# Kernel optimization log

Measured on AMD Instinct MI355X. Metric: run time of the kernel, lower is better.

The kernel has to match this reference:

```python
import jax, jax.numpy as jnp
import numpy as np
import math

EMBED_DIM = 768
NUM_HEADS = 12
HEAD_DIM = EMBED_DIM // NUM_HEADS
B, L = 8, 1024


def setup_inputs() -> dict:
    key = jax.random.key(0)
    ks = jax.random.split(key, 10)
    s = 1.0 / math.sqrt(EMBED_DIM)
    x = jax.random.normal(ks[0], (B, L, EMBED_DIM), dtype=jnp.float32)
    attention_mask = jnp.ones((B, L), dtype=jnp.int32)
    # torch nn.Linear weights: shape (out, in), y = x @ W.T + b
    Wq = jax.random.normal(ks[1], (EMBED_DIM, EMBED_DIM), jnp.float32) * s
    bq = jnp.zeros((EMBED_DIM,), jnp.float32)
    Wk = jax.random.normal(ks[2], (EMBED_DIM, EMBED_DIM), jnp.float32) * s
    bk = jnp.zeros((EMBED_DIM,), jnp.float32)
    Wv = jax.random.normal(ks[3], (EMBED_DIM, EMBED_DIM), jnp.float32) * s
    bv = jnp.zeros((EMBED_DIM,), jnp.float32)
    Wo = jax.random.normal(ks[4], (EMBED_DIM, EMBED_DIM), jnp.float32) * s
    bo = jnp.zeros((EMBED_DIM,), jnp.float32)
    return {"x": x, "attention_mask": attention_mask,
            "Wq": Wq, "bq": bq, "Wk": Wk, "bk": bk,
            "Wv": Wv, "bv": bv, "Wo": Wo, "bo": bo}


def reference(x, attention_mask, Wq, bq, Wk, bk, Wv, bv, Wo, bo):
    # NOTE: faithful to the original buggy forward:
    #   V = K_embed(x); scores = K @ K^T; Q unused; scale by sqrt(embed_dim);
    #   mask broadcasts over the KEY axis (masks entire query rows).
    b, l, d = x.shape
    K = x @ Wk.T + bk                                  # (B,L,D)
    Q = x @ Wq.T + bq                                  # computed but unused (as in source)
    V = K                                              # V = self.K_embed(x)
    Kh = K.reshape(b, l, NUM_HEADS, HEAD_DIM).transpose(0, 2, 1, 3)  # (B,H,L,dh)
    Vh = V.reshape(b, l, NUM_HEADS, HEAD_DIM).transpose(0, 2, 1, 3)
    scores = jnp.einsum('bhid,bhjd->bhij', Kh, Kh) / math.sqrt(EMBED_DIM)
    if attention_mask is not None:
        row_mask = attention_mask[:, None, :, None]    # (B,1,L,1) -> masks query rows
        scores = jnp.where(row_mask == 0, jnp.float32(-1e9), scores)
    attn = jax.nn.softmax(scores, axis=-1)             # dropout p=0 -> identity
    wV = jnp.einsum('bhij,bhjd->bhid', attn, Vh)       # (B,H,L,dh)
    wV = wV.transpose(0, 2, 1, 3).reshape(b, l, d)     # (B,L,D)
    out = wV @ Wo.T + bo
    return out
```

## Files before the change

kernel.cpp:

```cpp
#include <hip/hip_runtime.h>
#include <hip/hip_bf16.h>

#define NUM_B 8
#define SEQ 1024
#define DIM 768
#define NH 12
#define DH 64

typedef __attribute__((ext_vector_type(8))) short bf16x8;
typedef __attribute__((ext_vector_type(4))) float floatx4;
typedef __attribute__((ext_vector_type(4))) unsigned short ushortx4;
typedef __attribute__((ext_vector_type(8))) unsigned short ushortx8;

__device__ __forceinline__ unsigned short f2bf(float f) {
  unsigned u = __float_as_uint(f);
  u += 0x7FFFu + ((u >> 16) & 1u);
  return (unsigned short)(u >> 16);
}

#define GLOAD16(g, l) __builtin_amdgcn_global_load_lds( \
    (const __attribute__((address_space(1))) unsigned int*)(g), \
    (__attribute__((address_space(3))) unsigned int*)(l), 16, 0, 0)

__global__ __launch_bounds__(256) void convert_kernel(
    const float* __restrict__ x, const float* __restrict__ Wk,
    const float* __restrict__ Wo, unsigned short* __restrict__ xb,
    unsigned short* __restrict__ Wkb, unsigned short* __restrict__ Wob)
{
  const int NX4 = (8192 * 768) / 4;
  const int NW4 = (768 * 768) / 4;
  int i = blockIdx.x * 256 + threadIdx.x;
  const float* s; unsigned short* d; int off;
  if (i < NX4)            { s = x;  d = xb;  off = i; }
  else if (i < NX4 + NW4) { s = Wk; d = Wkb; off = i - NX4; }
  else                    { s = Wo; d = Wob; off = i - NX4 - NW4; }
  float4 v = ((const float4*)s)[off];
  ushortx4 h;
  h.x = f2bf(v.x); h.y = f2bf(v.y); h.z = f2bf(v.z); h.w = f2bf(v.w);
  ((ushortx4*)d)[off] = h;
}

__global__ __launch_bounds__(256) void proj_k_kernel(
    const unsigned short* __restrict__ xb, const unsigned short* __restrict__ Wkb,
    const float* __restrict__ bk, unsigned short* __restrict__ Kbh,
    unsigned short* __restrict__ KbhT)
{
  __shared__ __align__(16) unsigned short smem[24576];
  const int tid = threadIdx.x;
  const int lane = tid & 63;
  const int w = tid >> 6;
  const int wr = w >> 1, wc = w & 1;
  const int quad = lane >> 4, r16 = lane & 15;
  const int rs = r16 & 7;
  const int m0 = blockIdx.x * 64, n0 = blockIdx.y * 128;
  const int wbase = (tid & ~63);

  floatx4 acc[2][4] = {};

  auto stage = [&](int kt, int buf) {
    unsigned short* As = smem + buf * 12288;
    unsigned short* Bs = As + 4096;
#pragma unroll
    for (int i = 0; i < 2; ++i) {
      int c = tid + i * 256;
      int row = c >> 3, g = (c & 7) ^ (row & 7);
      GLOAD16(xb + (size_t)(m0 + row) * DIM + kt + g * 8,
              As + (size_t)(wbase + i * 256) * 8);
    }
#pragma unroll
    for (int i = 0; i < 4; ++i) {
      int c = tid + i * 256;
      int row = c >> 3, g = (c & 7) ^ (row & 7);
      GLOAD16(Wkb + (size_t)(n0 + row) * DIM + kt + g * 8,
              Bs + (size_t)(wbase + i * 256) * 8);
    }
  };

  stage(0, 0);
  int buf = 0;
  for (int it = 0; it < 12; ++it) {
    __syncthreads();
    if (it + 1 < 12) stage((it + 1) * 64, buf ^ 1);
    const unsigned short* As = smem + buf * 12288;
    const unsigned short* Bs = As + 4096;
    bf16x8 af[2][2], bfm[4][2];
#pragma unroll
    for (int mi = 0; mi < 2; ++mi)
#pragma unroll
      for (int kc = 0; kc < 2; ++kc)
        af[mi][kc] = *(const bf16x8*)&As[(wr * 32 + mi * 16 + r16) * 64 + ((kc * 4 + quad) ^ rs) * 8];
#pragma unroll
    for (int ni = 0; ni < 4; ++ni)
#pragma unroll
      for (int kc = 0; kc < 2; ++kc)
        bfm[ni][kc] = *(const bf16x8*)&Bs[(wc * 64 + ni * 16 + r16) * 64 + ((kc * 4 + quad) ^ rs) * 8];
#pragma unroll
    for (int mi = 0; mi < 2; ++mi)
#pragma unroll
      for (int ni = 0; ni < 4; ++ni) {
        acc[mi][ni] = __builtin_amdgcn_mfma_f32_16x16x32_bf16(af[mi][0], bfm[ni][0], acc[mi][ni], 0, 0, 0);
        acc[mi][ni] = __builtin_amdgcn_mfma_f32_16x16x32_bf16(af[mi][1], bfm[ni][1], acc[mi][ni], 0, 0, 0);
      }
    buf ^= 1;
  }

  __syncthreads();
  unsigned short* Ct = smem;
  const int bb = m0 >> 10, l0 = m0 & 1023;
#pragma unroll
  for (int mi = 0; mi < 2; ++mi)
#pragma unroll
    for (int ni = 0; ni < 4; ++ni) {
      int col = n0 + wc * 64 + ni * 16 + r16;
      float bias = bk[col];
      int hh = col >> 6, dd = col & 63;
      ushortx4 pk;
#pragma unroll
      for (int r = 0; r < 4; ++r) {
        int mrow = wr * 32 + mi * 16 + quad * 4 + r;
        unsigned short us = f2bf(acc[mi][ni][r] + bias);
        Kbh[((size_t)(bb * NH + hh) * SEQ + l0 + mrow) * DH + dd] = us;
        pk[r] = us;
      }
      *(ushortx4*)&Ct[(wc * 64 + ni * 16 + r16) * 72 + wr * 32 + mi * 16 + quad * 4] = pk;
    }
  __syncthreads();
#pragma unroll
  for (int i = 0; i < 4; ++i) {
    int c = tid + i * 256;
    int row = c >> 3, ch = c & 7;
    ushortx8 v = *(const ushortx8*)&Ct[row * 72 + ch * 8];
    int j = n0 + row;
    int hh = j >> 6, dd = j & 63;
    *(ushortx8*)&KbhT[((size_t)(bb * NH + hh) * DH + dd) * SEQ + l0 + ch * 8] = v;
  }
}

__global__ __launch_bounds__(256) void attn_kernel(
    const unsigned short* __restrict__ Kbh, const unsigned short* __restrict__ KbhT,
    const int* __restrict__ mask, unsigned short* __restrict__ wV)
{
  __shared__ __align__(16) unsigned short smem[25344];
  unsigned short* Ps = smem + 16384;
  float* rsum = (float*)&smem[25088];

  const int tid = threadIdx.x;
  const int lane = tid & 63;
  const int w = tid >> 6;
  const int quad = lane >> 4, r16 = lane & 15;
  const int rs = r16 & 7;
  const int qt = blockIdx.x, bh = blockIdx.y;
  const int b = bh / NH, h = bh % NH;
  const unsigned short* Kb  = Kbh  + (size_t)bh * SEQ * DH;
  const unsigned short* KbT = KbhT + (size_t)bh * DH * SEQ;
  const int q0 = qt * 128;
  const int qw = w * 32;
  const int wbase = (tid & ~63);
  const float SCALE = 0.036084391824351615f;

  bf16x8 aq[2][2];
#pragma unroll
  for (int nt = 0; nt < 2; ++nt)
#pragma unroll
    for (int kc = 0; kc < 2; ++kc)
      aq[nt][kc] = *(const bf16x8*)(Kb + (size_t)(q0 + qw + nt * 16 + r16) * DH + kc * 32 + quad * 8);

  float scm[2];
#pragma unroll
  for (int nt = 0; nt < 2; ++nt)
    scm[nt] = (mask[b * SEQ + q0 + qw + nt * 16 + r16] != 0) ? SCALE : 0.0f;

  floatx4 accO[2][4] = {};
  float psum[2] = {};

  auto stage = [&](int kt, int buf) {
    unsigned short* Ks  = smem + buf * 4096;
    unsigned short* KTs = smem + 8192 + buf * 4096;
#pragma unroll
    for (int i = 0; i < 2; ++i) {
      int c = tid + i * 256;
      int row = c >> 3, g = (c & 7) ^ (row & 7);
      GLOAD16(Kb + (size_t)(kt + row) * DH + g * 8,
              Ks + (size_t)(wbase + i * 256) * 8);
    }
#pragma unroll
    for (int i = 0; i < 2; ++i) {
      int c = tid + i * 256;
      int row = c >> 3, g = (c & 7) ^ (row & 7);
      GLOAD16(KbT + (size_t)row * SEQ + kt + g * 8,
              KTs + (size_t)(wbase + i * 256) * 8);
    }
  };

  stage(0, 0);
  int buf = 0;
  for (int it = 0; it < SEQ / 64; ++it) {
    __syncthreads();
    if (it + 1 < SEQ / 64) stage((it + 1) * 64, buf ^ 1);
    const unsigned short* Ks  = smem + buf * 4096;
    const unsigned short* KTs = smem + 8192 + buf * 4096;

    floatx4 St[4][2] = {};
#pragma unroll
    for (int kt = 0; kt < 4; ++kt) {
      int rb = (kt * 16 + r16) * 64;
      bf16x8 k0 = *(const bf16x8*)&Ks[rb + ((quad) ^ rs) * 8];
      bf16x8 k1 = *(const bf16x8*)&Ks[rb + ((4 + quad) ^ rs) * 8];
#pragma unroll
      for (int nt = 0; nt < 2; ++nt) {
        St[kt][nt] = __builtin_amdgcn_mfma_f32_16x16x32_bf16(k0, aq[nt][0], St[kt][nt], 0, 0, 0);
        St[kt][nt] = __builtin_amdgcn_mfma_f32_16x16x32_bf16(k1, aq[nt][1], St[kt][nt], 0, 0, 0);
      }
    }

#pragma unroll
    for (int nt = 0; nt < 2; ++nt) {
      float sc = scm[nt];
      int prow = (qw + nt * 16 + r16) * 68 + quad * 4;
#pragma unroll
      for (int kt = 0; kt < 4; ++kt) {
        float p0 = __expf(St[kt][nt][0] * sc);
        float p1 = __expf(St[kt][nt][1] * sc);
        float p2 = __expf(St[kt][nt][2] * sc);
        float p3 = __expf(St[kt][nt][3] * sc);
        psum[nt] += (p0 + p1) + (p2 + p3);
        __hip_bfloat162 lo = __float22bfloat162_rn(make_float2(p0, p1));
        __hip_bfloat162 hi = __float22bfloat162_rn(make_float2(p2, p3));
        unsigned u0, u1;
        __builtin_memcpy(&u0, &lo, 4);
        __builtin_memcpy(&u1, &hi, 4);
        *(uint2*)&Ps[prow + kt * 16] = make_uint2(u0, u1);
      }
    }

    bf16x8 ap[2][2];
#pragma unroll
    for (int mi = 0; mi < 2; ++mi)
#pragma unroll
      for (int kc = 0; kc < 2; ++kc)
        ap[mi][kc] = *(const bf16x8*)&Ps[(qw + mi * 16 + r16) * 68 + kc * 32 + quad * 8];
#pragma unroll
    for (int ni = 0; ni < 4; ++ni) {
      int rb = (ni * 16 + r16) * 64;
      bf16x8 v0 = *(const bf16x8*)&KTs[rb + ((quad) ^ rs) * 8];
      bf16x8 v1 = *(const bf16x8*)&KTs[rb + ((4 + quad) ^ rs) * 8];
#pragma unroll
      for (int mi = 0; mi < 2; ++mi) {
        accO[mi][ni] = __builtin_amdgcn_mfma_f32_16x16x32_bf16(ap[mi][0], v0, accO[mi][ni], 0, 0, 0);
        accO[mi][ni] = __builtin_amdgcn_mfma_f32_16x16x32_bf16(ap[mi][1], v1, accO[mi][ni], 0, 0, 0);
      }
    }
    buf ^= 1;
  }

#pragma unroll
  for (int nt = 0; nt < 2; ++nt) {
    float s = psum[nt];
    s += __shfl_xor(s, 16);
    s += __shfl_xor(s, 32);
    psum[nt] = s;
  }
  if (quad == 0) {
#pragma unroll
    for (int nt = 0; nt < 2; ++nt)
      rsum[qw + nt * 16 + r16] = psum[nt];
  }
  float rinv[2][4];
#pragma unroll
  for (int mi = 0; mi < 2; ++mi)
#pragma unroll
    for (int r = 0; r < 4; ++r)
      rinv[mi][r] = 1.0f / rsum[qw + mi * 16 + quad * 4 + r];

#pragma unroll
  for (int mi = 0; mi < 2; ++mi)
#pragma unroll
    for (int ni = 0; ni < 4; ++ni)
#pragma unroll
      for (int r = 0; r < 4; ++r) {
        int l = q0 + qw + mi * 16 + quad * 4 + r;
        int col = h * DH + ni * 16 + r16;
        wV[(size_t)(b * SEQ + l) * DIM + col] = f2bf(accO[mi][ni][r] * rinv[mi][r]);
      }
}

__global__ __launch_bounds__(256) void proj_o_kernel(
    const unsigned short* __restrict__ wVb, const unsigned short* __restrict__ Wob,
    const float* __restrict__ bo, float* __restrict__ out)
{
  __shared__ __align__(16) unsigned short smem[24576];
  const int tid = threadIdx.x;
  const int lane = tid & 63;
  const int w = tid >> 6;
  const int wr = w >> 1, wc = w & 1;
  const int quad = lane >> 4, r16 = lane & 15;
  const int rs = r16 & 7;
  const int m0 = blockIdx.x * 64, n0 = blockIdx.y * 128;
  const int wbase = (tid & ~63);

  floatx4 acc[2][4] = {};

  auto stage = [&](int kt, int buf) {
    unsigned short* As = smem + buf * 12288;
    unsigned short* Bs = As + 4096;
#pragma unroll
    for (int i = 0; i < 2; ++i) {
      int c = tid + i * 256;
      int row = c >> 3, g = (c & 7) ^ (row & 7);
      GLOAD16(wVb + (size_t)(m0 + row) * DIM + kt + g * 8,
              As + (size_t)(wbase + i * 256) * 8);
    }
#pragma unroll
    for (int i = 0; i < 4; ++i) {
      int c = tid + i * 256;
      int row = c >> 3, g = (c & 7) ^ (row & 7);
      GLOAD16(Wob + (size_t)(n0 + row) * DIM + kt + g * 8,
              Bs + (size_t)(wbase + i * 256) * 8);
    }
  };

  stage(0, 0);
  int buf = 0;
  for (int it = 0; it < 12; ++it) {
    __syncthreads();
    if (it + 1 < 12) stage((it + 1) * 64, buf ^ 1);
    const unsigned short* As = smem + buf * 12288;
    const unsigned short* Bs = As + 4096;
    bf16x8 af[2][2], bfm[4][2];
#pragma unroll
    for (int mi = 0; mi < 2; ++mi)
#pragma unroll
      for (int kc = 0; kc < 2; ++kc)
        af[mi][kc] = *(const bf16x8*)&As[(wr * 32 + mi * 16 + r16) * 64 + ((kc * 4 + quad) ^ rs) * 8];
#pragma unroll
    for (int ni = 0; ni < 4; ++ni)
#pragma unroll
      for (int kc = 0; kc < 2; ++kc)
        bfm[ni][kc] = *(const bf16x8*)&Bs[(wc * 64 + ni * 16 + r16) * 64 + ((kc * 4 + quad) ^ rs) * 8];
#pragma unroll
    for (int mi = 0; mi < 2; ++mi)
#pragma unroll
      for (int ni = 0; ni < 4; ++ni) {
        acc[mi][ni] = __builtin_amdgcn_mfma_f32_16x16x32_bf16(af[mi][0], bfm[ni][0], acc[mi][ni], 0, 0, 0);
        acc[mi][ni] = __builtin_amdgcn_mfma_f32_16x16x32_bf16(af[mi][1], bfm[ni][1], acc[mi][ni], 0, 0, 0);
      }
    buf ^= 1;
  }

#pragma unroll
  for (int mi = 0; mi < 2; ++mi)
#pragma unroll
    for (int ni = 0; ni < 4; ++ni) {
      int col = n0 + wc * 64 + ni * 16 + r16;
      float bias = bo[col];
#pragma unroll
      for (int r = 0; r < 4; ++r) {
        int row = m0 + wr * 32 + mi * 16 + quad * 4 + r;
        out[(size_t)row * DIM + col] = acc[mi][ni][r] + bias;
      }
    }
}

extern "C" void kernel_launch(void* const* d_in, const int* in_sizes, int n_in,
                              void* d_out, int out_size, void* d_ws, size_t ws_size,
                              hipStream_t stream) {
  const float* x  = (const float*)d_in[0];
  const int* mask = (const int*)d_in[1];
  const float* Wk = (const float*)d_in[4];
  const float* bk = (const float*)d_in[5];
  const float* Wo = (const float*)d_in[8];
  const float* bo = (const float*)d_in[9];
  float* out = (float*)d_out;

  unsigned short* p = (unsigned short*)d_ws;
  unsigned short* xb   = p;  p += (size_t)8192 * 768;
  unsigned short* Wkb  = p;  p += (size_t)768 * 768;
  unsigned short* Wob  = p;  p += (size_t)768 * 768;
  unsigned short* Kbh  = p;  p += (size_t)NUM_B * NH * SEQ * DH;
  unsigned short* KbhT = p;  p += (size_t)NUM_B * NH * SEQ * DH;
  unsigned short* wVb  = p;

  convert_kernel<<<7296, 256, 0, stream>>>(x, Wk, Wo, xb, Wkb, Wob);
  proj_k_kernel<<<dim3(128, 6), 256, 0, stream>>>(xb, Wkb, bk, Kbh, KbhT);
  attn_kernel<<<dim3(8, NUM_B * NH), 256, 0, stream>>>(Kbh, KbhT, mask, wVb);
  proj_o_kernel<<<dim3(128, 6), 256, 0, stream>>>(wVb, Wob, bo, out);
}
```

Baseline: 184.0 us.

## Split attention block across 8 waves with 16 query rows each, use exp2

The attention kernel now launches 512 threads per block. Each of 8 waves handles 16 query rows instead of 32, and each thread stages one 16-byte chunk per tile instead of two. The softmax scale is premultiplied by log2(e) so the exponent can use the hardware exp2 instruction directly. This is meant to add wave-level parallelism for latency hiding and cut register pressure. In exchange, each wave now reuses every K/KT tile read from shared memory for half as many query rows, and barrier cost grows with more waves per block.

Measured after the change: 174.5 us. 5.2% less time.

```diff
diff --git a/kernel.cpp b/kernel.cpp
--- a/kernel.cpp
+++ b/kernel.cpp
@@ -136,7 +136,7 @@
   }
 }
 
-__global__ __launch_bounds__(256) void attn_kernel(
+__global__ __launch_bounds__(512) void attn_kernel(
     const unsigned short* __restrict__ Kbh, const unsigned short* __restrict__ KbhT,
     const int* __restrict__ mask, unsigned short* __restrict__ wV)
 {
@@ -154,42 +154,28 @@
   const unsigned short* Kb  = Kbh  + (size_t)bh * SEQ * DH;
   const unsigned short* KbT = KbhT + (size_t)bh * DH * SEQ;
   const int q0 = qt * 128;
-  const int qw = w * 32;
+  const int qw = w * 16;
   const int wbase = (tid & ~63);
-  const float SCALE = 0.036084391824351615f;
-
-  bf16x8 aq[2][2];
-#pragma unroll
-  for (int nt = 0; nt < 2; ++nt)
-#pragma unroll
-    for (int kc = 0; kc < 2; ++kc)
-      aq[nt][kc] = *(const bf16x8*)(Kb + (size_t)(q0 + qw + nt * 16 + r16) * DH + kc * 32 + quad * 8);
-
-  float scm[2];
-#pragma unroll
-  for (int nt = 0; nt < 2; ++nt)
-    scm[nt] = (mask[b * SEQ + q0 + qw + nt * 16 + r16] != 0) ? SCALE : 0.0f;
-
-  floatx4 accO[2][4] = {};
-  float psum[2] = {};
+  const float SCALE2 = 0.036084391824351615f * 1.4426950408889634f;
+
+  bf16x8 aq[2];
+#pragma unroll
+  for (int kc = 0; kc < 2; ++kc)
+    aq[kc] = *(const bf16x8*)(Kb + (size_t)(q0 + qw + r16) * DH + kc * 32 + quad * 8);
+
+  const float scm = (mask[b * SEQ + q0 + qw + r16] != 0) ? SCALE2 : 0.0f;
+
+  floatx4 accO[4] = {};
+  float psum = 0.0f;
 
   auto stage = [&](int kt, int buf) {
     unsigned short* Ks  = smem + buf * 4096;
     unsigned short* KTs = smem + 8192 + buf * 4096;
-#pragma unroll
-    for (int i = 0; i < 2; ++i) {
-      int c = tid + i * 256;
-      int row = c >> 3, g = (c & 7) ^ (row & 7);
-      GLOAD16(Kb + (size_t)(kt + row) * DH + g * 8,
-              Ks + (size_t)(wbase + i * 256) * 8);
-    }
-#pragma unroll
-    for (int i = 0; i < 2; ++i) {
-      int c = tid + i * 256;
-      int row = c >> 3, g = (c & 7) ^ (row & 7);
-      GLOAD16(KbT + (size_t)row * SEQ + kt + g * 8,
-              KTs + (size_t)(wbase + i * 256) * 8);
-    }
+    int row = tid >> 3, g = (tid & 7) ^ (row & 7);
+    GLOAD16(Kb + (size_t)(kt + row) * DH + g * 8,
+            Ks + (size_t)wbase * 8);
+    GLOAD16(KbT + (size_t)row * SEQ + kt + g * 8,
+            KTs + (size_t)wbase * 8);
   };
 
   stage(0, 0);
@@ -200,30 +186,25 @@
     const unsigned short* Ks  = smem + buf * 4096;
     const unsigned short* KTs = smem + 8192 + buf * 4096;
 
-    floatx4 St[4][2] = {};
+    floatx4 St[4] = {};
 #pragma unroll
     for (int kt = 0; kt < 4; ++kt) {
       int rb = (kt * 16 + r16) * 64;
       bf16x8 k0 = *(const bf16x8*)&Ks[rb + ((quad) ^ rs) * 8];
       bf16x8 k1 = *(const bf16x8*)&Ks[rb + ((4 + quad) ^ rs) * 8];
-#pragma unroll
-      for (int nt = 0; nt < 2; ++nt) {
-        St[kt][nt] = __builtin_amdgcn_mfma_f32_16x16x32_bf16(k0, aq[nt][0], St[kt][nt], 0, 0, 0);
-        St[kt][nt] = __builtin_amdgcn_mfma_f32_16x16x32_bf16(k1, aq[nt][1], St[kt][nt], 0, 0, 0);
-      }
-    }
-
-#pragma unroll
-    for (int nt = 0; nt < 2; ++nt) {
-      float sc = scm[nt];
-      int prow = (qw + nt * 16 + r16) * 68 + quad * 4;
+      St[kt] = __builtin_amdgcn_mfma_f32_16x16x32_bf16(k0, aq[0], St[kt], 0, 0, 0);
+      St[kt] = __builtin_amdgcn_mfma_f32_16x16x32_bf16(k1, aq[1], St[kt], 0, 0, 0);
+    }
+
+    {
+      int prow = (qw + r16) * 68 + quad * 4;
 #pragma unroll
       for (int kt = 0; kt < 4; ++kt) {
-        float p0 = __expf(St[kt][nt][0] * sc);
-        float p1 = __expf(St[kt][nt][1] * sc);
-        float p2 = __expf(St[kt][nt][2] * sc);
-        float p3 = __expf(St[kt][nt][3] * sc);
-        psum[nt] += (p0 + p1) + (p2 + p3);
+        float p0 = __builtin_amdgcn_exp2f(St[kt][0] * scm);
+        float p1 = __builtin_amdgcn_exp2f(St[kt][1] * scm);
+        float p2 = __builtin_amdgcn_exp2f(St[kt][2] * scm);
+        float p3 = __builtin_amdgcn_exp2f(St[kt][3] * scm);
+        psum += (p0 + p1) + (p2 + p3);
         __hip_bfloat162 lo = __float22bfloat162_rn(make_float2(p0, p1));
         __hip_bfloat162 hi = __float22bfloat162_rn(make_float2(p2, p3));
         unsigned u0, u1;
@@ -233,55 +214,40 @@
       }
     }
 
-    bf16x8 ap[2][2];
-#pragma unroll
-    for (int mi = 0; mi < 2; ++mi)
-#pragma unroll
-      for (int kc = 0; kc < 2; ++kc)
-        ap[mi][kc] = *(const bf16x8*)&Ps[(qw + mi * 16 + r16) * 68 + kc * 32 + quad * 8];
+    bf16x8 ap[2];
+#pragma unroll
+    for (int kc = 0; kc < 2; ++kc)
+      ap[kc] = *(const bf16x8*)&Ps[(qw + r16) * 68 + kc * 32 + quad * 8];
 #pragma unroll
     for (int ni = 0; ni < 4; ++ni) {
       int rb = (ni * 16 + r16) * 64;
       bf16x8 v0 = *(const bf16x8*)&KTs[rb + ((quad) ^ rs) * 8];
       bf16x8 v1 = *(const bf16x8*)&KTs[rb + ((4 + quad) ^ rs) * 8];
-#pragma unroll
-      for (int mi = 0; mi < 2; ++mi) {
-        accO[mi][ni] = __builtin_amdgcn_mfma_f32_16x16x32_bf16(ap[mi][0], v0, accO[mi][ni], 0, 0, 0);
-        accO[mi][ni] = __builtin_amdgcn_mfma_f32_16x16x32_bf16(ap[mi][1], v1, accO[mi][ni], 0, 0, 0);
-      }
+      accO[ni] = __builtin_amdgcn_mfma_f32_16x16x32_bf16(ap[0], v0, accO[ni], 0, 0, 0);
+      accO[ni] = __builtin_amdgcn_mfma_f32_16x16x32_bf16(ap[1], v1, accO[ni], 0, 0, 0);
     }
     buf ^= 1;
   }
 
-#pragma unroll
-  for (int nt = 0; nt < 2; ++nt) {
-    float s = psum[nt];
+  {
+    float s = psum;
     s += __shfl_xor(s, 16);
     s += __shfl_xor(s, 32);
-    psum[nt] = s;
-  }
-  if (quad == 0) {
-#pragma unroll
-    for (int nt = 0; nt < 2; ++nt)
-      rsum[qw + nt * 16 + r16] = psum[nt];
-  }
-  float rinv[2][4];
-#pragma unroll
-  for (int mi = 0; mi < 2; ++mi)
-#pragma unroll
-    for (int r = 0; r < 4; ++r)
-      rinv[mi][r] = 1.0f / rsum[qw + mi * 16 + quad * 4 + r];
-
-#pragma unroll
-  for (int mi = 0; mi < 2; ++mi)
-#pragma unroll
-    for (int ni = 0; ni < 4; ++ni)
-#pragma unroll
-      for (int r = 0; r < 4; ++r) {
-        int l = q0 + qw + mi * 16 + quad * 4 + r;
-        int col = h * DH + ni * 16 + r16;
-        wV[(size_t)(b * SEQ + l) * DIM + col] = f2bf(accO[mi][ni][r] * rinv[mi][r]);
-      }
+    if (quad == 0) rsum[qw + r16] = s;
+  }
+  float rinv[4];
+#pragma unroll
+  for (int r = 0; r < 4; ++r)
+    rinv[r] = 1.0f / rsum[qw + quad * 4 + r];
+
+#pragma unroll
+  for (int ni = 0; ni < 4; ++ni)
+#pragma unroll
+    for (int r = 0; r < 4; ++r) {
+      int l = q0 + qw + quad * 4 + r;
+      int col = h * DH + ni * 16 + r16;
+      wV[(size_t)(b * SEQ + l) * DIM + col] = f2bf(accO[ni][r] * rinv[r]);
+    }
 }
 
 __global__ __launch_bounds__(256) void proj_o_kernel(
@@ -382,6 +348,6 @@
 
   convert_kernel<<<7296, 256, 0, stream>>>(x, Wk, Wo, xb, Wkb, Wob);
   proj_k_kernel<<<dim3(128, 6), 256, 0, stream>>>(xb, Wkb, bk, Kbh, KbhT);
-  attn_kernel<<<dim3(8, NUM_B * NH), 256, 0, stream>>>(Kbh, KbhT, mask, wVb);
+  attn_kernel<<<dim3(8, NUM_B * NH), 512, 0, stream>>>(Kbh, KbhT, mask, wVb);
   proj_o_kernel<<<dim3(128, 6), 256, 0, stream>>>(wVb, Wob, bo, out);
 }
```

## Enlarge attention blocks to 256 queries with 512 threads and remap grid

Applied to the files above, without the earlier changes.

The attention kernel now runs 8 waves per block, each covering 32 queries, so one block handles 256 query rows. Every staged K/K^T tile is therefore shared by twice as many queries, and each thread issues one staged load per matrix instead of two. The grid becomes 1D and is remapped so that neighbouring blocks work on different heads. Exponentials use exp2 with log2(e) folded into the scale, and s_setprio raises wave priority around the MFMA sections. The cost is a larger LDS footprint and fewer, bigger blocks (384), which may lower occupancy or leave the CUs less evenly loaded.

After: 183.9 us. No clear change (-0.1%).

```diff
diff --git a/kernel.cpp b/kernel.cpp
--- a/kernel.cpp
+++ b/kernel.cpp
@@ -136,27 +136,34 @@
   }
 }
 
-__global__ __launch_bounds__(256) void attn_kernel(
+__global__ __launch_bounds__(512) void attn_kernel(
     const unsigned short* __restrict__ Kbh, const unsigned short* __restrict__ KbhT,
     const int* __restrict__ mask, unsigned short* __restrict__ wV)
 {
-  __shared__ __align__(16) unsigned short smem[25344];
+  __shared__ __align__(16) unsigned short smem[34304];
   unsigned short* Ps = smem + 16384;
-  float* rsum = (float*)&smem[25088];
+  float* rsum = (float*)&smem[33792];
 
   const int tid = threadIdx.x;
   const int lane = tid & 63;
   const int w = tid >> 6;
   const int quad = lane >> 4, r16 = lane & 15;
   const int rs = r16 & 7;
-  const int qt = blockIdx.x, bh = blockIdx.y;
+  const int Lb = blockIdx.x;
+  const int qt = (Lb >> 3) & 3;
+  const int bh = (Lb >> 5) * 8 + (Lb & 7);
   const int b = bh / NH, h = bh % NH;
   const unsigned short* Kb  = Kbh  + (size_t)bh * SEQ * DH;
   const unsigned short* KbT = KbhT + (size_t)bh * DH * SEQ;
-  const int q0 = qt * 128;
+  const int q0 = qt * 256;
   const int qw = w * 32;
   const int wbase = (tid & ~63);
-  const float SCALE = 0.036084391824351615f;
+  const float SCALE2 = 0.036084391824351615f * 1.4426950408889634f;
+
+  float scm[2];
+#pragma unroll
+  for (int nt = 0; nt < 2; ++nt)
+    scm[nt] = (mask[b * SEQ + q0 + qw + nt * 16 + r16] != 0) ? SCALE2 : 0.0f;
 
   bf16x8 aq[2][2];
 #pragma unroll
@@ -164,11 +171,6 @@
 #pragma unroll
     for (int kc = 0; kc < 2; ++kc)
       aq[nt][kc] = *(const bf16x8*)(Kb + (size_t)(q0 + qw + nt * 16 + r16) * DH + kc * 32 + quad * 8);
-
-  float scm[2];
-#pragma unroll
-  for (int nt = 0; nt < 2; ++nt)
-    scm[nt] = (mask[b * SEQ + q0 + qw + nt * 16 + r16] != 0) ? SCALE : 0.0f;
 
   floatx4 accO[2][4] = {};
   float psum[2] = {};
@@ -176,20 +178,11 @@
   auto stage = [&](int kt, int buf) {
     unsigned short* Ks  = smem + buf * 4096;
     unsigned short* KTs = smem + 8192 + buf * 4096;
-#pragma unroll
-    for (int i = 0; i < 2; ++i) {
-      int c = tid + i * 256;
-      int row = c >> 3, g = (c & 7) ^ (row & 7);
-      GLOAD16(Kb + (size_t)(kt + row) * DH + g * 8,
-              Ks + (size_t)(wbase + i * 256) * 8);
-    }
-#pragma unroll
-    for (int i = 0; i < 2; ++i) {
-      int c = tid + i * 256;
-      int row = c >> 3, g = (c & 7) ^ (row & 7);
-      GLOAD16(KbT + (size_t)row * SEQ + kt + g * 8,
-              KTs + (size_t)(wbase + i * 256) * 8);
-    }
+    int row = tid >> 3, g = (tid & 7) ^ (row & 7);
+    GLOAD16(Kb + (size_t)(kt + row) * DH + g * 8,
+            Ks + (size_t)wbase * 8);
+    GLOAD16(KbT + (size_t)row * SEQ + kt + g * 8,
+            KTs + (size_t)wbase * 8);
   };
 
   stage(0, 0);
@@ -201,6 +194,7 @@
     const unsigned short* KTs = smem + 8192 + buf * 4096;
 
     floatx4 St[4][2] = {};
+    __builtin_amdgcn_s_setprio(1);
 #pragma unroll
     for (int kt = 0; kt < 4; ++kt) {
       int rb = (kt * 16 + r16) * 64;
@@ -212,6 +206,7 @@
         St[kt][nt] = __builtin_amdgcn_mfma_f32_16x16x32_bf16(k1, aq[nt][1], St[kt][nt], 0, 0, 0);
       }
     }
+    __builtin_amdgcn_s_setprio(0);
 
 #pragma unroll
     for (int nt = 0; nt < 2; ++nt) {
@@ -219,10 +214,10 @@
       int prow = (qw + nt * 16 + r16) * 68 + quad * 4;
 #pragma unroll
       for (int kt = 0; kt < 4; ++kt) {
-        float p0 = __expf(St[kt][nt][0] * sc);
-        float p1 = __expf(St[kt][nt][1] * sc);
-        float p2 = __expf(St[kt][nt][2] * sc);
-        float p3 = __expf(St[kt][nt][3] * sc);
+        float p0 = __builtin_amdgcn_exp2f(St[kt][nt][0] * sc);
+        float p1 = __builtin_amdgcn_exp2f(St[kt][nt][1] * sc);
+        float p2 = __builtin_amdgcn_exp2f(St[kt][nt][2] * sc);
+        float p3 = __builtin_amdgcn_exp2f(St[kt][nt][3] * sc);
         psum[nt] += (p0 + p1) + (p2 + p3);
         __hip_bfloat162 lo = __float22bfloat162_rn(make_float2(p0, p1));
         __hip_bfloat162 hi = __float22bfloat162_rn(make_float2(p2, p3));
@@ -239,6 +234,7 @@
 #pragma unroll
       for (int kc = 0; kc < 2; ++kc)
         ap[mi][kc] = *(const bf16x8*)&Ps[(qw + mi * 16 + r16) * 68 + kc * 32 + quad * 8];
+    __builtin_amdgcn_s_setprio(1);
 #pragma unroll
     for (int ni = 0; ni < 4; ++ni) {
       int rb = (ni * 16 + r16) * 64;
@@ -250,6 +246,7 @@
         accO[mi][ni] = __builtin_amdgcn_mfma_f32_16x16x32_bf16(ap[mi][1], v1, accO[mi][ni], 0, 0, 0);
       }
     }
+    __builtin_amdgcn_s_setprio(0);
     buf ^= 1;
   }
 
@@ -382,6 +379,6 @@
 
   convert_kernel<<<7296, 256, 0, stream>>>(x, Wk, Wo, xb, Wkb, Wob);
   proj_k_kernel<<<dim3(128, 6), 256, 0, stream>>>(xb, Wkb, bk, Kbh, KbhT);
-  attn_kernel<<<dim3(8, NUM_B * NH), 256, 0, stream>>>(Kbh, KbhT, mask, wVb);
+  attn_kernel<<<384, 512, 0, stream>>>(Kbh, KbhT, mask, wVb);
   proj_o_kernel<<<dim3(128, 6), 256, 0, stream>>>(wVb, Wob, bo, out);
 }
```
